# Kernel tuning notes

Hardware: AMD Instinct MI355X
Metric: run time of the kernel (lower is better)

## Reference

```python
import jax, jax.numpy as jnp
import numpy as np

B, P, D = 128, 196, 2048      # batch, num_pixels (14*14), encoder_dim
A, E, H, V = 512, 512, 512, 10000  # attention_dim, embedding_size, lstm_size, vocab
T_MAX = 20
T = T_MAX - 1                 # decoder steps = max_length - 1


def setup_inputs() -> dict:
    key = jax.random.key(0)
    ks = jax.random.split(key, 24)
    s = lambda k, sh: (jax.random.normal(k, sh, jnp.float32) * 0.02)
    features = jax.random.normal(ks[0], (B, P, D), jnp.float32)
    captions = jax.random.randint(ks[1], (B, T_MAX), 0, V)
    # sorted-descending ragged lengths in [4, T_MAX]; force max to T_MAX
    lengths = jnp.sort(jax.random.randint(ks[2], (B,), 4, T_MAX + 1))[::-1].at[0].set(T_MAX)
    return dict(
        features=features, captions=captions, lengths=lengths,
        emb=s(ks[3], (V, E)),
        h_fc_w=s(ks[4], (D, H)), h_fc_b=jnp.zeros((H,), jnp.float32),
        c_fc_w=s(ks[5], (D, H)), c_fc_b=jnp.zeros((H,), jnp.float32),
        enc_w=s(ks[6], (D, A)), enc_b=jnp.zeros((A,), jnp.float32),
        dec_w=s(ks[7], (H, A)), dec_b=jnp.zeros((A,), jnp.float32),
        att_w=s(ks[8], (A, 1)), att_b=jnp.zeros((1,), jnp.float32),
        beta_w=s(ks[9], (H, D)), beta_b=jnp.zeros((D,), jnp.float32),
        w_ih=s(ks[10], (D + E, 4 * H)), b_ih=jnp.zeros((4 * H,), jnp.float32),
        w_hh=s(ks[11], (H, 4 * H)), b_hh=jnp.zeros((4 * H,), jnp.float32),
        cls_w=s(ks[12], (H, V)), cls_b=jnp.zeros((V,), jnp.float32),
    )


def reference(features, captions, lengths, emb,
              h_fc_w, h_fc_b, c_fc_w, c_fc_b,
              enc_w, enc_b, dec_w, dec_b, att_w, att_b,
              beta_w, beta_b, w_ih, b_ih, w_hh, b_hh, cls_w, cls_b):
    dec_len = lengths - 1                       # decoder_lengths
    mean_f = features.mean(axis=1)              # [B, D]
    h = mean_f @ h_fc_w + h_fc_b                # [B, H]
    c = mean_f @ c_fc_w + c_fc_b
    att1 = features @ enc_w + enc_b             # [B, P, A] (loop-invariant)
    emb_seq = emb[captions[:, :T]]              # [B, T, E]
    xs = (jnp.moveaxis(emb_seq, 0, 1),          # [T, B, E]
          jnp.arange(T)[:, None] < dec_len[None, :])  # [T, B] step-valid mask

    def step(carry, x):
        h, c = carry
        e_t, m = x                              # [B, E], [B] bool
        att2 = h @ dec_w + dec_b                # [B, A]
        e = jnp.squeeze(jax.nn.relu(att1 + att2[:, None, :]) @ att_w + att_b, -1)  # [B, P]
        alpha = jax.nn.softmax(e, axis=1)
        awe = jnp.einsum('bp,bpd->bd', alpha, features)
        gate = jax.nn.sigmoid(h @ beta_w + beta_b)
        awe = gate * awe
        xin = jnp.concatenate([e_t, awe], axis=1)           # [B, E+D]
        gates = xin @ w_ih + b_ih + h @ w_hh + b_hh         # [B, 4H]
        i, f, g, o = jnp.split(gates, 4, axis=1)
        c_new = jax.nn.sigmoid(f) * c + jax.nn.sigmoid(i) * jnp.tanh(g)
        h_new = jax.nn.sigmoid(o) * jnp.tanh(c_new)
        mf = m[:, None].astype(h.dtype)
        y = (h_new @ cls_w + cls_b) * mf        # rows past their length stay 0
        h = jnp.where(m[:, None], h_new, h)
        c = jnp.where(m[:, None], c_new, c)
        return (h, c), (y, alpha * mf)

    _, (ys, alphas) = jax.lax.scan(step, (h, c), xs)
    y_predicted = jnp.moveaxis(ys, 0, 1)        # [B, T, V]
    alphas = jnp.moveaxis(alphas, 0, 1)         # [B, T, P]
    return y_predicted, alphas
```

## Files before the change

### kernel.cpp

```cpp
#include <hip/hip_runtime.h>
#include <cstdint>
#include <cstddef>


#define DEV __device__ __forceinline__

typedef __attribute__((ext_vector_type(8))) short s16x8;
typedef __attribute__((ext_vector_type(4))) float f32x4;

constexpr int Bb = 128, Pp = 196, Dd = 2048, Aa = 512, Ee = 512, Hh = 512, Vv = 10000;
constexpr int Tt = 19, TMAX = 20;
constexpr int KXN = 2560;
constexpr int NVP = 10048;

DEV float fbs(short s) {
    union { uint32_t u; float f; } v;
    v.u = ((uint32_t)(uint16_t)s) << 16;
    return v.f;
}
DEV short bfs(float f) {
    union { float f; uint32_t u; } v;
    v.f = f;
    uint32_t u = v.u;
    uint32_t r = (u + 0x7FFFu + ((u >> 16) & 1u)) >> 16;
    return (short)(uint16_t)r;
}

template<int BM, int BN, int BK, int WR, int WC>
DEV void tile_mm(const short* __restrict__ Ag, int lda,
                 const short* __restrict__ Bg, int ldb, int K,
                 int m0, int n0, char* smem,
                 f32x4 (&acc)[(BM / WR) / 16][(BN / WC) / 16])
{
    constexpr int TH = 256;
    constexpr int NCH = BK / 8, AU = NCH * BM, BU = NCH * BN;
    constexpr int APT = AU / TH, BPT = BU / TH;
    constexpr int WM = BM / WR, WN = BN / WC, FM = WM / 16, FN = WN / 16;
    short* sA = (short*)smem;
    short* sB = (short*)smem + AU * 8;
    const int tid = threadIdx.x, lane = tid & 63, wid = tid >> 6;
    const int l15 = lane & 15, l4 = lane >> 4, wr = wid / WC, wc = wid % WC;

    #pragma unroll
    for (int i = 0; i < FM; ++i)
        #pragma unroll
        for (int j = 0; j < FN; ++j) acc[i][j] = {0.f, 0.f, 0.f, 0.f};

    for (int kt = 0; kt < K; kt += BK) {
        s16x8 ra[APT], rb[BPT];
        #pragma unroll
        for (int i = 0; i < APT; ++i) {
            int q2 = tid + TH * i;
            int r2 = q2 / NCH, ch = q2 % NCH;
            ra[i] = *(const s16x8*)(Ag + (size_t)(m0 + r2) * lda + kt + ch * 8);
        }
        #pragma unroll
        for (int i = 0; i < BPT; ++i) {
            int q2 = tid + TH * i;
            int r2 = q2 / NCH, ch = q2 % NCH;
            rb[i] = *(const s16x8*)(Bg + (size_t)(n0 + r2) * ldb + kt + ch * 8);
        }
        __syncthreads();
        #pragma unroll
        for (int i = 0; i < APT; ++i) {
            int q2 = tid + TH * i;
            int r2 = q2 / NCH, ch = q2 % NCH;
            *(s16x8*)(sA + (r2 * NCH + (ch ^ (r2 & 7))) * 8) = ra[i];
        }
        #pragma unroll
        for (int i = 0; i < BPT; ++i) {
            int q2 = tid + TH * i;
            int r2 = q2 / NCH, ch = q2 % NCH;
            *(s16x8*)(sB + (r2 * NCH + (ch ^ (r2 & 7))) * 8) = rb[i];
        }
        __syncthreads();
        #pragma unroll
        for (int ks = 0; ks < BK / 32; ++ks) {
            s16x8 af[FM], bf[FN];
            #pragma unroll
            for (int fm = 0; fm < FM; ++fm) {
                int rr2 = wr * WM + fm * 16 + l15, cc = ks * 4 + l4;
                af[fm] = *(const s16x8*)&sA[(rr2 * NCH + (cc ^ (rr2 & 7))) * 8];
            }
            #pragma unroll
            for (int fn = 0; fn < FN; ++fn) {
                int rr2 = wc * WN + fn * 16 + l15, cc = ks * 4 + l4;
                bf[fn] = *(const s16x8*)&sB[(rr2 * NCH + (cc ^ (rr2 & 7))) * 8];
            }
            #pragma unroll
            for (int fm = 0; fm < FM; ++fm)
                #pragma unroll
                for (int fn = 0; fn < FN; ++fn)
                    acc[fm][fn] = __builtin_amdgcn_mfma_f32_16x16x32_bf16(af[fm], bf[fn], acc[fm][fn], 0, 0, 0);
        }
        __syncthreads();
    }
}

template<int BM, int BN, int BK, int TH, int WR, int WC, int EPI>
__global__ __launch_bounds__(TH) void gemm_k(
    const short* __restrict__ Ag, int lda,
    const short* __restrict__ Bg, int ldb,
    int K,
    float* __restrict__ outF, float* __restrict__ outF2,
    short* __restrict__ outH, short* __restrict__ outH2,
    int ldo,
    const float* __restrict__ bias, const float* __restrict__ bias2,
    const int* __restrict__ lens)
{
    constexpr int NCH = BK / 8;
    constexpr int AU = NCH * BM, BU = NCH * BN;
    constexpr int APT = AU / TH, BPT = BU / TH;
    constexpr int WM = BM / WR, WN = BN / WC;
    constexpr int FM = WM / 16, FN = WN / 16;

    __shared__ __align__(16) short sA[AU * 8];
    __shared__ __align__(16) short sB[BU * 8];

    const int tid = threadIdx.x, lane = tid & 63, wid = tid >> 6;
    const int l15 = lane & 15, l4 = lane >> 4;

    int m0, n0, trow_ = 0;
    if constexpr (EPI == 0) {
        int task = (blockIdx.x & 7) * 49 + (blockIdx.x >> 3);
        m0 = (task >> 1) * BM;
        n0 = (task & 1) * BN;
    } else if constexpr (EPI == 3) {
        const int nwg = (int)gridDim.x;
        const int qq = nwg >> 3, rr = nwg & 7;
        int xcd = (int)blockIdx.x & 7, idx = (int)blockIdx.x >> 3;
        int task = (xcd < rr) ? xcd * (qq + 1) + idx
                              : rr * (qq + 1) + (xcd - rr) * qq + idx;
        int npanel = task / Tt;
        trow_ = task - npanel * Tt;
        m0 = trow_ * BM;
        n0 = npanel * BN;
    } else if constexpr (EPI == 4) {
        m0 = ((int)blockIdx.x & 3) * BM;
        n0 = ((int)blockIdx.x >> 2) * BN;
    } else {
        m0 = blockIdx.y * BM;
        n0 = blockIdx.x * BN;
    }
    const int wr = wid / WC, wc = wid % WC;

    f32x4 acc[FM][FN];
    #pragma unroll
    for (int i = 0; i < FM; ++i)
        #pragma unroll
        for (int j = 0; j < FN; ++j) acc[i][j] = {0.f, 0.f, 0.f, 0.f};

    for (int kt = 0; kt < K; kt += BK) {
        s16x8 ra[APT], rb[BPT];
        #pragma unroll
        for (int i = 0; i < APT; ++i) {
            int q2 = tid + TH * i;
            int r2 = q2 / NCH, ch = q2 % NCH;
            ra[i] = *(const s16x8*)(Ag + (size_t)(m0 + r2) * lda + kt + ch * 8);
        }
        #pragma unroll
        for (int i = 0; i < BPT; ++i) {
            int q2 = tid + TH * i;
            int r2 = q2 / NCH, ch = q2 % NCH;
            rb[i] = *(const s16x8*)(Bg + (size_t)(n0 + r2) * ldb + kt + ch * 8);
        }
        __syncthreads();
        #pragma unroll
        for (int i = 0; i < APT; ++i) {
            int q2 = tid + TH * i;
            int r2 = q2 / NCH, ch = q2 % NCH;
            *(s16x8*)(sA + (r2 * NCH + (ch ^ (r2 & 7))) * 8) = ra[i];
        }
        #pragma unroll
        for (int i = 0; i < BPT; ++i) {
            int q2 = tid + TH * i;
            int r2 = q2 / NCH, ch = q2 % NCH;
            *(s16x8*)(sB + (r2 * NCH + (ch ^ (r2 & 7))) * 8) = rb[i];
        }
        __syncthreads();
        #pragma unroll
        for (int ks = 0; ks < BK / 32; ++ks) {
            s16x8 af[FM], bf[FN];
            #pragma unroll
            for (int fm = 0; fm < FM; ++fm) {
                int rr2 = wr * WM + fm * 16 + l15, cc = ks * 4 + l4;
                af[fm] = *(const s16x8*)&sA[(rr2 * NCH + (cc ^ (rr2 & 7))) * 8];
            }
            #pragma unroll
            for (int fn = 0; fn < FN; ++fn) {
                int rr2 = wc * WN + fn * 16 + l15, cc = ks * 4 + l4;
                bf[fn] = *(const s16x8*)&sB[(rr2 * NCH + (cc ^ (rr2 & 7))) * 8];
            }
            #pragma unroll
            for (int fm = 0; fm < FM; ++fm)
                #pragma unroll
                for (int fn = 0; fn < FN; ++fn)
                    acc[fm][fn] = __builtin_amdgcn_mfma_f32_16x16x32_bf16(af[fm], bf[fn], acc[fm][fn], 0, 0, 0);
        }
        __syncthreads();
    }

    #pragma unroll
    for (int fm = 0; fm < FM; ++fm)
        #pragma unroll
        for (int fn = 0; fn < FN; ++fn)
            #pragma unroll
            for (int r2 = 0; r2 < 4; ++r2) {
                int ml = wr * WM + fm * 16 + l4 * 4 + r2;
                int nl = wc * WN + fn * 16 + l15;
                int m = m0 + ml, n = n0 + nl;
                float v = acc[fm][fn][r2];
                if constexpr (EPI == 0) {
                    outH[(size_t)m * ldo + n] = bfs(v + bias[n]);
                } else if constexpr (EPI == 1) {
                    outH[(size_t)m * ldo + n] = bfs(v);
                } else if constexpr (EPI == 3) {
                    if (n < Vv) {
                        bool mk = trow_ < lens[ml] - 1;
                        outF[((size_t)ml * Tt + trow_) * Vv + n] = mk ? (v + bias[n]) : 0.f;
                    }
                } else if constexpr (EPI == 4) {
                    if (n < 512) outF[(size_t)m * Aa + n] = v + bias[n];
                    else outF2[(size_t)m * Dd + (n - 512)] =
                             1.f / (1.f + expf(-(v + bias2[n - 512])));
                } else if constexpr (EPI == 6) {
                    if (n < 512) {
                        outH2[(size_t)m * KXN + 2048 + n] = bfs(v + bias[n]);
                    } else {
                        outF2[(size_t)m * 512 + (n - 512)] = v + bias2[n - 512];
                    }
                }
            }
}

__global__ __launch_bounds__(512) void att_awe_k(
    const short* __restrict__ att1b, const float* __restrict__ att2b,
    const float* __restrict__ att_w, const float* __restrict__ att_b,
    const short* __restrict__ featb, const float* __restrict__ gatebuf,
    short* __restrict__ xin, float* __restrict__ al_out,
    const int* __restrict__ lens, int t)
{
    const int b = blockIdx.y, half = blockIdx.x;
    const int tid = threadIdx.x, lane = tid & 63, wid = tid >> 6;
    __shared__ float se[224];
    __shared__ float sred[256];
    __shared__ float sal[224];

    float aw[8], a2[8];
    #pragma unroll
    for (int j = 0; j < 8; ++j) {
        aw[j] = att_w[lane * 8 + j];
        a2[j] = att2b[b * 512 + lane * 8 + j];
    }
    float ab = att_b[0];
    for (int p = wid; p < Pp; p += 8) {
        s16x8 row = *(const s16x8*)&att1b[((size_t)b * Pp + p) * 512 + lane * 8];
        float s = 0.f;
        #pragma unroll
        for (int j = 0; j < 8; ++j) {
            float v = fbs(row[j]) + a2[j];
            v = v > 0.f ? v : 0.f;
            s += v * aw[j];
        }
        #pragma unroll
        for (int m = 32; m; m >>= 1) s += __shfl_xor(s, m);
        if (lane == 0) se[p] = s + ab;
    }
    __syncthreads();
    float e = 0.f, ex = 0.f;
    if (tid < 256) {
        e = (tid < Pp) ? se[tid] : -3.0e38f;
        sred[tid] = e;
    }
    __syncthreads();
    for (int st = 128; st > 0; st >>= 1) {
        if (tid < st) sred[tid] = fmaxf(sred[tid], sred[tid + st]);
        __syncthreads();
    }
    float mx = sred[0];
    __syncthreads();
    if (tid < 256) {
        ex = (tid < Pp) ? expf(e - mx) : 0.f;
        sred[tid] = ex;
    }
    __syncthreads();
    for (int st = 128; st > 0; st >>= 1) {
        if (tid < st) sred[tid] += sred[tid + st];
        __syncthreads();
    }
    float inv = 1.f / sred[0];
    if (tid < Pp) {
        float al = ex * inv;
        sal[tid] = al;
        if (half == 0) {
            float mf = (t < lens[b] - 1) ? 1.f : 0.f;
            al_out[((size_t)b * Tt + t) * Pp + tid] = al * mf;
        }
    }
    __syncthreads();
    int d0 = half * 1024 + tid * 2;
    const short* f = featb + (size_t)b * Pp * Dd + d0;
    float s0 = 0.f, s1 = 0.f;
    #pragma unroll 4
    for (int p = 0; p < Pp; ++p) {
        uint32_t v = *(const uint32_t*)(f + (size_t)p * Dd);
        float al = sal[p];
        s0 += al * fbs((short)(v & 0xFFFF));
        s1 += al * fbs((short)(v >> 16));
    }
    float2 g = *(const float2*)&gatebuf[b * 2048 + d0];
    uint32_t o = ((uint32_t)(uint16_t)bfs(g.y * s1) << 16) | (uint16_t)bfs(g.x * s0);
    *(uint32_t*)(xin + (size_t)b * KXN + d0) = o;
}

__global__ __launch_bounds__(256) void gates_lstm_k(
    const short* __restrict__ xin, const short* __restrict__ combT,
    const short* __restrict__ eprec,
    const float* __restrict__ b_ih, const float* __restrict__ b_hh,
    float* __restrict__ c_state, short* __restrict__ hnew_all,
    short* __restrict__ xin_h, const int* __restrict__ lens, int t)
{
    __shared__ __align__(16) char smem[16384];
    int m0 = ((int)blockIdx.x & 3) * 32, n0 = ((int)blockIdx.x >> 2) * 32;
    f32x4 acc[1][1];
    tile_mm<32, 32, 128, 2, 2>(xin, KXN, combT, KXN, KXN, m0, n0, smem, acc);
    int tid = threadIdx.x, lane = tid & 63, wid = tid >> 6;
    int l15 = lane & 15, l4 = lane >> 4, wr = wid / 2, wc = wid % 2;
    float* sE = (float*)smem;
    #pragma unroll
    for (int r = 0; r < 4; ++r) {
        int ml = wr * 16 + l4 * 4 + r, nl = wc * 16 + l15;
        sE[ml * 32 + nl] = acc[0][0][r];
    }
    __syncthreads();
    int bl = tid >> 3, jl = tid & 7;
    int b = m0 + bl, q = (n0 >> 2) + jl;
    f32x4 ge = *(const f32x4*)&sE[bl * 32 + jl * 4];
    short4 ep = *(const short4*)&eprec[((size_t)t * 128 + b) * 2048 + n0 + jl * 4];
    float gi = ge[0] + fbs(ep.x) + b_ih[q]        + b_hh[q];
    float gf = ge[1] + fbs(ep.y) + b_ih[512 + q]  + b_hh[512 + q];
    float gg = ge[2] + fbs(ep.z) + b_ih[1024 + q] + b_hh[1024 + q];
    float go = ge[3] + fbs(ep.w) + b_ih[1536 + q] + b_hh[1536 + q];
    float si = 1.f / (1.f + expf(-gi));
    float sf = 1.f / (1.f + expf(-gf));
    float so = 1.f / (1.f + expf(-go));
    float tg = tanhf(gg);
    int sidx = b * 512 + q;
    float cn = sf * c_state[sidx] + si * tg;
    float hn = so * tanhf(cn);
    hnew_all[((size_t)t * 128 + b) * 512 + q] = bfs(hn);
    if (t < lens[b] - 1) {
        c_state[sidx] = cn;
        xin_h[(size_t)b * KXN + 2048 + q] = bfs(hn);
    }
}

__global__ __launch_bounds__(256) void conv_mean_k(
    const float* __restrict__ feat, short* __restrict__ featb, short* __restrict__ meanb)
{
    int b = blockIdx.y;
    int d = (blockIdx.x * 256 + threadIdx.x) * 4;
    const float* f = feat + (size_t)b * Pp * Dd + d;
    short* o = featb + (size_t)b * Pp * Dd + d;
    float s0 = 0.f, s1 = 0.f, s2 = 0.f, s3 = 0.f;
    for (int p = 0; p < Pp; ++p) {
        float4 v = *(const float4*)(f + (size_t)p * Dd);
        s0 += v.x; s1 += v.y; s2 += v.z; s3 += v.w;
        short4 ov = make_short4(bfs(v.x), bfs(v.y), bfs(v.z), bfs(v.w));
        *(short4*)(o + (size_t)p * Dd) = ov;
    }
    const float inv = 1.f / 196.f;
    short4 mv = make_short4(bfs(s0 * inv), bfs(s1 * inv), bfs(s2 * inv), bfs(s3 * inv));
    *(short4*)(meanb + (size_t)b * Dd + d) = mv;
}

template<int PERM>
__global__ __launch_bounds__(256) void transpose_bf16(
    const float* __restrict__ src, int R, int C,
    short* __restrict__ dst, int dstStride, int colOff, int Cpad)
{
    __shared__ float tile[32][33];
    int c0 = blockIdx.x * 32, r0 = blockIdx.y * 32;
    int tx = threadIdx.x & 31, ty = threadIdx.x >> 5;
    #pragma unroll
    for (int i = 0; i < 4; ++i) {
        int r = r0 + ty + i * 8, c = c0 + tx;
        tile[ty + i * 8][tx] = (r < R && c < C) ? src[(size_t)r * C + c] : 0.f;
    }
    __syncthreads();
    #pragma unroll
    for (int i = 0; i < 4; ++i) {
        int cc = c0 + ty + i * 8, rr = r0 + tx;
        if (cc < Cpad && rr < R) {
            int drow = PERM ? ((cc & 511) * 4 + (cc >> 9)) : cc;
            dst[(size_t)drow * dstStride + colOff + rr] = bfs(tile[tx][ty + i * 8]);
        }
    }
}

__global__ __launch_bounds__(256) void embg_k(
    const float* __restrict__ emb, const int* __restrict__ caps, short* __restrict__ embseq)
{
    size_t i = (size_t)blockIdx.x * 256 + threadIdx.x;
    if (i >= (size_t)Tt * Bb * Ee) return;
    int e = (int)(i % Ee);
    size_t r = i / Ee;
    int b = (int)(r % Bb);
    int t = (int)(r / Bb);
    int cap = caps[b * TMAX + t];
    embseq[i] = bfs(emb[(size_t)cap * Ee + e]);
}

extern "C" void kernel_launch(void* const* d_in, const int* in_sizes, int n_in,
                              void* d_out, int out_size, void* d_ws, size_t ws_size,
                              hipStream_t stream)
{
    const float* features = (const float*)d_in[0];
    const int* captions   = (const int*)d_in[1];
    const int* lengths    = (const int*)d_in[2];
    const float* emb      = (const float*)d_in[3];
    const float* h_fc_w   = (const float*)d_in[4];
    const float* h_fc_b   = (const float*)d_in[5];
    const float* c_fc_w   = (const float*)d_in[6];
    const float* c_fc_b   = (const float*)d_in[7];
    const float* enc_w    = (const float*)d_in[8];
    const float* enc_b    = (const float*)d_in[9];
    const float* dec_w    = (const float*)d_in[10];
    const float* dec_b    = (const float*)d_in[11];
    const float* att_w    = (const float*)d_in[12];
    const float* att_b    = (const float*)d_in[13];
    const float* beta_w   = (const float*)d_in[14];
    const float* beta_b   = (const float*)d_in[15];
    const float* w_ih     = (const float*)d_in[16];
    const float* b_ih     = (const float*)d_in[17];
    const float* w_hh     = (const float*)d_in[18];
    const float* b_hh     = (const float*)d_in[19];
    const float* cls_w    = (const float*)d_in[20];
    const float* cls_b    = (const float*)d_in[21];

    char* w = (char*)d_ws;
    auto alloc = [&](size_t bytes) {
        char* p = w;
        w += (bytes + 255) & ~(size_t)255;
        return p;
    };
    short* featb    = (short*)alloc((size_t)Bb * Pp * Dd * 2);
    short* att1b    = (short*)alloc((size_t)Bb * Pp * Aa * 2);
    short* encT     = (short*)alloc((size_t)Aa * Dd * 2);
    short* combT    = (short*)alloc((size_t)2048 * KXN * 2);
    short* wtopT    = (short*)alloc((size_t)2048 * 512 * 2);
    short* clsT     = (short*)alloc((size_t)NVP * Hh * 2);
    short* catT     = (short*)alloc((size_t)2560 * Hh * 2);
    short* hcT      = (short*)alloc((size_t)1024 * Dd * 2);
    short* embseq   = (short*)alloc((size_t)Tt * Bb * Ee * 2);
    short* meanb    = (short*)alloc((size_t)Bb * Dd * 2);
    short* eprec    = (short*)alloc((size_t)Tt * Bb * 2048 * 2);
    float* c_state  = (float*)alloc((size_t)Bb * Hh * 4);
    float* att2b    = (float*)alloc((size_t)Bb * Aa * 4);
    float* gatebuf  = (float*)alloc((size_t)Bb * Dd * 4);
    short* xin      = (short*)alloc((size_t)Bb * KXN * 2);
    short* hnew_all = (short*)alloc((size_t)Tt * Bb * Hh * 2);

    float* y_out  = (float*)d_out;
    float* al_out = y_out + (size_t)Bb * Tt * Vv;

    conv_mean_k<<<dim3(2, 128), 256, 0, stream>>>(features, featb, meanb);
    transpose_bf16<0><<<dim3(16, 64), 256, 0, stream>>>(enc_w, 2048, 512, encT, 2048, 0, 512);
    transpose_bf16<0><<<dim3(16, 64), 256, 0, stream>>>(h_fc_w, 2048, 512, hcT, 2048, 0, 512);
    transpose_bf16<0><<<dim3(16, 64), 256, 0, stream>>>(c_fc_w, 2048, 512, hcT + (size_t)512 * 2048, 2048, 0, 512);
    transpose_bf16<0><<<dim3(16, 16), 256, 0, stream>>>(dec_w, 512, 512, catT, 512, 0, 512);
    transpose_bf16<0><<<dim3(64, 16), 256, 0, stream>>>(beta_w, 512, 2048, catT + (size_t)512 * 512, 512, 0, 2048);
    transpose_bf16<1><<<dim3(64, 64), 256, 0, stream>>>(w_ih + (size_t)512 * 2048, 2048, 2048, combT, KXN, 0, 2048);
    transpose_bf16<1><<<dim3(64, 16), 256, 0, stream>>>(w_hh, 512, 2048, combT, KXN, 2048, 2048);
    transpose_bf16<1><<<dim3(64, 16), 256, 0, stream>>>(w_ih, 512, 2048, wtopT, 512, 0, 2048);
    transpose_bf16<0><<<dim3(314, 16), 256, 0, stream>>>(cls_w, 512, 10000, clsT, 512, 0, NVP);
    embg_k<<<(Tt * Bb * Ee + 255) / 256, 256, 0, stream>>>(emb, captions, embseq);

    gemm_k<128, 64, 64, 256, 2, 2, 6><<<dim3(16, 1), 256, 0, stream>>>(
        meanb, 2048, hcT, 2048, 2048,
        nullptr, c_state, nullptr, xin, 0, h_fc_b, c_fc_b, nullptr);

    gemm_k<128, 256, 64, 512, 2, 4, 0><<<dim3(392), 512, 0, stream>>>(
        featb, 2048, encT, 2048, 2048,
        nullptr, nullptr, att1b, nullptr, Aa, enc_b, nullptr, nullptr);

    gemm_k<128, 64, 64, 256, 2, 2, 1><<<dim3(32, 19), 256, 0, stream>>>(
        embseq, 512, wtopT, 512, 512,
        nullptr, nullptr, eprec, nullptr, 2048, nullptr, nullptr, nullptr);

    for (int t = 0; t < Tt; ++t) {
        gemm_k<32, 64, 64, 256, 2, 2, 4><<<dim3(160), 256, 0, stream>>>(
            xin + 2048, KXN, catT, 512, 512,
            att2b, gatebuf, nullptr, nullptr, 0, dec_b, beta_b, nullptr);
        att_awe_k<<<dim3(2, 128), 512, 0, stream>>>(
            att1b, att2b, att_w, att_b, featb, gatebuf, xin,
            al_out, lengths, t);
        gates_lstm_k<<<dim3(256), 256, 0, stream>>>(
            xin, combT, eprec, b_ih, b_hh, c_state, hnew_all, xin, lengths, t);
    }

    gemm_k<128, 64, 64, 256, 2, 2, 3><<<dim3(157 * Tt), 256, 0, stream>>>(
        hnew_all, 512, clsT, 512, 512,
        y_out, nullptr, nullptr, nullptr, 0, cls_b, nullptr, lengths);
}
```

Before: 1.475 ms.

## Fuse att2/gate GEMV into attention kernel, merge prep transposes, pipeline LSTM GEMM

The per-step att2/beta-gate GEMM launch is removed. Each attention block now computes its own h·dec_w and sigmoid(h·beta_w) slice as a scalar GEMV from the bf16 weights, cutting one launch per step and the att2/gate round trip through global memory. In exchange, each of the two half-blocks per batch row recomputes the full att2 vector, and every block reads weight rows redundantly. The LSTM gates GEMM gets a hand-written double-buffered register prefetch. The many weight-transpose and embedding-gather launches are merged into a single prep kernel, and the feature conversion now uses narrower per-thread vectors across more blocks.

```diff
diff --git a/kernel.cpp b/kernel.cpp
--- a/kernel.cpp
+++ b/kernel.cpp
@@ -7,6 +7,7 @@
 
 typedef __attribute__((ext_vector_type(8))) short s16x8;
 typedef __attribute__((ext_vector_type(4))) float f32x4;
+typedef __attribute__((ext_vector_type(4))) unsigned int u32x4;
 
 constexpr int Bb = 128, Pp = 196, Dd = 2048, Aa = 512, Ee = 512, Hh = 512, Vv = 10000;
 constexpr int Tt = 19, TMAX = 20;
@@ -25,76 +26,12 @@
     uint32_t r = (u + 0x7FFFu + ((u >> 16) & 1u)) >> 16;
     return (short)(uint16_t)r;
 }
-
-template<int BM, int BN, int BK, int WR, int WC>
-DEV void tile_mm(const short* __restrict__ Ag, int lda,
-                 const short* __restrict__ Bg, int ldb, int K,
-                 int m0, int n0, char* smem,
-                 f32x4 (&acc)[(BM / WR) / 16][(BN / WC) / 16])
-{
-    constexpr int TH = 256;
-    constexpr int NCH = BK / 8, AU = NCH * BM, BU = NCH * BN;
-    constexpr int APT = AU / TH, BPT = BU / TH;
-    constexpr int WM = BM / WR, WN = BN / WC, FM = WM / 16, FN = WN / 16;
-    short* sA = (short*)smem;
-    short* sB = (short*)smem + AU * 8;
-    const int tid = threadIdx.x, lane = tid & 63, wid = tid >> 6;
-    const int l15 = lane & 15, l4 = lane >> 4, wr = wid / WC, wc = wid % WC;
-
-    #pragma unroll
-    for (int i = 0; i < FM; ++i)
-        #pragma unroll
-        for (int j = 0; j < FN; ++j) acc[i][j] = {0.f, 0.f, 0.f, 0.f};
-
-    for (int kt = 0; kt < K; kt += BK) {
-        s16x8 ra[APT], rb[BPT];
-        #pragma unroll
-        for (int i = 0; i < APT; ++i) {
-            int q2 = tid + TH * i;
-            int r2 = q2 / NCH, ch = q2 % NCH;
-            ra[i] = *(const s16x8*)(Ag + (size_t)(m0 + r2) * lda + kt + ch * 8);
-        }
-        #pragma unroll
-        for (int i = 0; i < BPT; ++i) {
-            int q2 = tid + TH * i;
-            int r2 = q2 / NCH, ch = q2 % NCH;
-            rb[i] = *(const s16x8*)(Bg + (size_t)(n0 + r2) * ldb + kt + ch * 8);
-        }
-        __syncthreads();
-        #pragma unroll
-        for (int i = 0; i < APT; ++i) {
-            int q2 = tid + TH * i;
-            int r2 = q2 / NCH, ch = q2 % NCH;
-            *(s16x8*)(sA + (r2 * NCH + (ch ^ (r2 & 7))) * 8) = ra[i];
-        }
-        #pragma unroll
-        for (int i = 0; i < BPT; ++i) {
-            int q2 = tid + TH * i;
-            int r2 = q2 / NCH, ch = q2 % NCH;
-            *(s16x8*)(sB + (r2 * NCH + (ch ^ (r2 & 7))) * 8) = rb[i];
-        }
-        __syncthreads();
-        #pragma unroll
-        for (int ks = 0; ks < BK / 32; ++ks) {
-            s16x8 af[FM], bf[FN];
-            #pragma unroll
-            for (int fm = 0; fm < FM; ++fm) {
-                int rr2 = wr * WM + fm * 16 + l15, cc = ks * 4 + l4;
-                af[fm] = *(const s16x8*)&sA[(rr2 * NCH + (cc ^ (rr2 & 7))) * 8];
-            }
-            #pragma unroll
-            for (int fn = 0; fn < FN; ++fn) {
-                int rr2 = wc * WN + fn * 16 + l15, cc = ks * 4 + l4;
-                bf[fn] = *(const s16x8*)&sB[(rr2 * NCH + (cc ^ (rr2 & 7))) * 8];
-            }
-            #pragma unroll
-            for (int fm = 0; fm < FM; ++fm)
-                #pragma unroll
-                for (int fn = 0; fn < FN; ++fn)
-                    acc[fm][fn] = __builtin_amdgcn_mfma_f32_16x16x32_bf16(af[fm], bf[fn], acc[fm][fn], 0, 0, 0);
-        }
-        __syncthreads();
-    }
+DEV void upk(uint32_t v, float& lo, float& hi) {
+    union { uint32_t u; float f; } a, b;
+    a.u = v << 16;
+    b.u = v & 0xffff0000u;
+    lo = a.f;
+    hi = b.f;
 }
 
 template<int BM, int BN, int BK, int TH, int WR, int WC, int EPI>
@@ -135,9 +72,6 @@
         trow_ = task - npanel * Tt;
         m0 = trow_ * BM;
         n0 = npanel * BN;
-    } else if constexpr (EPI == 4) {
-        m0 = ((int)blockIdx.x & 3) * BM;
-        n0 = ((int)blockIdx.x >> 2) * BN;
     } else {
         m0 = blockIdx.y * BM;
         n0 = blockIdx.x * BN;
@@ -219,10 +153,6 @@
                         bool mk = trow_ < lens[ml] - 1;
                         outF[((size_t)ml * Tt + trow_) * Vv + n] = mk ? (v + bias[n]) : 0.f;
                     }
-                } else if constexpr (EPI == 4) {
-                    if (n < 512) outF[(size_t)m * Aa + n] = v + bias[n];
-                    else outF2[(size_t)m * Dd + (n - 512)] =
-                             1.f / (1.f + expf(-(v + bias2[n - 512])));
                 } else if constexpr (EPI == 6) {
                     if (n < 512) {
                         outH2[(size_t)m * KXN + 2048 + n] = bfs(v + bias[n]);
@@ -234,83 +164,124 @@
 }
 
 __global__ __launch_bounds__(512) void att_awe_k(
-    const short* __restrict__ att1b, const float* __restrict__ att2b,
+    const short* __restrict__ att1b, const short* __restrict__ catT,
+    const float* __restrict__ dec_b, const float* __restrict__ beta_b,
     const float* __restrict__ att_w, const float* __restrict__ att_b,
-    const short* __restrict__ featb, const float* __restrict__ gatebuf,
-    short* __restrict__ xin, float* __restrict__ al_out,
-    const int* __restrict__ lens, int t)
+    const short* __restrict__ featb, short* __restrict__ xin,
+    float* __restrict__ al_out, const int* __restrict__ lens, int t)
 {
     const int b = blockIdx.y, half = blockIdx.x;
     const int tid = threadIdx.x, lane = tid & 63, wid = tid >> 6;
+    __shared__ float sh[512];
+    __shared__ float sa2[512];
     __shared__ float se[224];
     __shared__ float sred[256];
     __shared__ float sal[224];
 
-    float aw[8], a2[8];
-    #pragma unroll
-    for (int j = 0; j < 8; ++j) {
-        aw[j] = att_w[lane * 8 + j];
-        a2[j] = att2b[b * 512 + lane * 8 + j];
-    }
-    float ab = att_b[0];
-    for (int p = wid; p < Pp; p += 8) {
-        s16x8 row = *(const s16x8*)&att1b[((size_t)b * Pp + p) * 512 + lane * 8];
-        float s = 0.f;
+    if (tid < 256) {
+        uint32_t v = ((const uint32_t*)(xin + (size_t)b * KXN + 2048))[tid];
+        float lo, hi;
+        upk(v, lo, hi);
+        sh[tid * 2] = lo;
+        sh[tid * 2 + 1] = hi;
+    }
+    __syncthreads();
+
+    const int d0 = half * 1024 + tid * 2;
+    {
+        const short* wa = catT + (size_t)tid * 512;
+        const short* w0 = catT + (size_t)(512 + d0) * 512;
+        const short* w1 = w0 + 512;
+        float accA = 0.f, acc0 = 0.f, acc1 = 0.f;
+        #pragma unroll 4
+        for (int k = 0; k < 512; k += 8) {
+            u32x4 va = *(const u32x4*)(wa + k);
+            u32x4 v0 = *(const u32x4*)(w0 + k);
+            u32x4 v1 = *(const u32x4*)(w1 + k);
+            float hv[8];
+            *(float4*)&hv[0] = *(const float4*)&sh[k];
+            *(float4*)&hv[4] = *(const float4*)&sh[k + 4];
+            #pragma unroll
+            for (int j = 0; j < 4; ++j) {
+                float lo, hi;
+                upk(va[j], lo, hi); accA += lo * hv[2 * j] + hi * hv[2 * j + 1];
+                upk(v0[j], lo, hi); acc0 += lo * hv[2 * j] + hi * hv[2 * j + 1];
+                upk(v1[j], lo, hi); acc1 += lo * hv[2 * j] + hi * hv[2 * j + 1];
+            }
+        }
+        sa2[tid] = accA + dec_b[tid];
+        float g0 = 1.f / (1.f + expf(-(acc0 + beta_b[d0])));
+        float g1 = 1.f / (1.f + expf(-(acc1 + beta_b[d0 + 1])));
+        __syncthreads();
+
+        float aw[8], a2[8];
         #pragma unroll
         for (int j = 0; j < 8; ++j) {
-            float v = fbs(row[j]) + a2[j];
-            v = v > 0.f ? v : 0.f;
-            s += v * aw[j];
-        }
-        #pragma unroll
-        for (int m = 32; m; m >>= 1) s += __shfl_xor(s, m);
-        if (lane == 0) se[p] = s + ab;
-    }
-    __syncthreads();
-    float e = 0.f, ex = 0.f;
-    if (tid < 256) {
-        e = (tid < Pp) ? se[tid] : -3.0e38f;
-        sred[tid] = e;
-    }
-    __syncthreads();
-    for (int st = 128; st > 0; st >>= 1) {
-        if (tid < st) sred[tid] = fmaxf(sred[tid], sred[tid + st]);
-        __syncthreads();
-    }
-    float mx = sred[0];
-    __syncthreads();
-    if (tid < 256) {
-        ex = (tid < Pp) ? expf(e - mx) : 0.f;
-        sred[tid] = ex;
-    }
-    __syncthreads();
-    for (int st = 128; st > 0; st >>= 1) {
-        if (tid < st) sred[tid] += sred[tid + st];
-        __syncthreads();
-    }
-    float inv = 1.f / sred[0];
-    if (tid < Pp) {
-        float al = ex * inv;
-        sal[tid] = al;
-        if (half == 0) {
-            float mf = (t < lens[b] - 1) ? 1.f : 0.f;
-            al_out[((size_t)b * Tt + t) * Pp + tid] = al * mf;
-        }
-    }
-    __syncthreads();
-    int d0 = half * 1024 + tid * 2;
-    const short* f = featb + (size_t)b * Pp * Dd + d0;
-    float s0 = 0.f, s1 = 0.f;
-    #pragma unroll 4
-    for (int p = 0; p < Pp; ++p) {
-        uint32_t v = *(const uint32_t*)(f + (size_t)p * Dd);
-        float al = sal[p];
-        s0 += al * fbs((short)(v & 0xFFFF));
-        s1 += al * fbs((short)(v >> 16));
-    }
-    float2 g = *(const float2*)&gatebuf[b * 2048 + d0];
-    uint32_t o = ((uint32_t)(uint16_t)bfs(g.y * s1) << 16) | (uint16_t)bfs(g.x * s0);
-    *(uint32_t*)(xin + (size_t)b * KXN + d0) = o;
+            aw[j] = att_w[lane * 8 + j];
+            a2[j] = sa2[lane * 8 + j];
+        }
+        float ab = att_b[0];
+        for (int p = wid; p < Pp; p += 8) {
+            s16x8 row = *(const s16x8*)&att1b[((size_t)b * Pp + p) * 512 + lane * 8];
+            float s = 0.f;
+            #pragma unroll
+            for (int j = 0; j < 8; ++j) {
+                float v = fbs(row[j]) + a2[j];
+                v = v > 0.f ? v : 0.f;
+                s += v * aw[j];
+            }
+            #pragma unroll
+            for (int m = 32; m; m >>= 1) s += __shfl_xor(s, m);
+            if (lane == 0) se[p] = s + ab;
+        }
+        __syncthreads();
+
+        float e = 0.f, ex = 0.f;
+        if (tid < 256) {
+            e = (tid < Pp) ? se[tid] : -3.0e38f;
+            sred[tid] = e;
+        }
+        __syncthreads();
+        for (int st = 128; st > 0; st >>= 1) {
+            if (tid < st) sred[tid] = fmaxf(sred[tid], sred[tid + st]);
+            __syncthreads();
+        }
+        float mx = sred[0];
+        __syncthreads();
+        if (tid < 256) {
+            ex = (tid < Pp) ? expf(e - mx) : 0.f;
+            sred[tid] = ex;
+        }
+        __syncthreads();
+        for (int st = 128; st > 0; st >>= 1) {
+            if (tid < st) sred[tid] += sred[tid + st];
+            __syncthreads();
+        }
+        float inv = 1.f / sred[0];
+        if (tid < Pp) {
+            float al = ex * inv;
+            sal[tid] = al;
+            if (half == 0) {
+                float mf = (t < lens[b] - 1) ? 1.f : 0.f;
+                al_out[((size_t)b * Tt + t) * Pp + tid] = al * mf;
+            }
+        }
+        __syncthreads();
+
+        const short* f = featb + (size_t)b * Pp * Dd + d0;
+        float s0 = 0.f, s1 = 0.f;
+        #pragma unroll 4
+        for (int p = 0; p < Pp; ++p) {
+            uint32_t v = *(const uint32_t*)(f + (size_t)p * Dd);
+            float lo, hi;
+            upk(v, lo, hi);
+            float al = sal[p];
+            s0 += al * lo;
+            s1 += al * hi;
+        }
+        uint32_t o = ((uint32_t)(uint16_t)bfs(g1 * s1) << 16) | (uint16_t)bfs(g0 * s0);
+        *(uint32_t*)(xin + (size_t)b * KXN + d0) = o;
+    }
 }
 
 __global__ __launch_bounds__(256) void gates_lstm_k(
@@ -320,17 +291,71 @@
     float* __restrict__ c_state, short* __restrict__ hnew_all,
     short* __restrict__ xin_h, const int* __restrict__ lens, int t)
 {
-    __shared__ __align__(16) char smem[16384];
-    int m0 = ((int)blockIdx.x & 3) * 32, n0 = ((int)blockIdx.x >> 2) * 32;
-    f32x4 acc[1][1];
-    tile_mm<32, 32, 128, 2, 2>(xin, KXN, combT, KXN, KXN, m0, n0, smem, acc);
-    int tid = threadIdx.x, lane = tid & 63, wid = tid >> 6;
-    int l15 = lane & 15, l4 = lane >> 4, wr = wid / 2, wc = wid % 2;
-    float* sE = (float*)smem;
+    constexpr int BM = 32, BN = 32, BK = 128, K = KXN;
+    constexpr int NCH = BK / 8;
+    constexpr int AU = NCH * BM;
+    __shared__ __align__(16) short sA[AU * 8];
+    __shared__ __align__(16) short sB[AU * 8];
+
+    const int m0 = ((int)blockIdx.x & 3) * BM, n0 = ((int)blockIdx.x >> 2) * BN;
+    const int tid = threadIdx.x, lane = tid & 63, wid = tid >> 6;
+    const int l15 = lane & 15, l4 = lane >> 4;
+    const int wr = wid >> 1, wc = wid & 1;
+
+    f32x4 acc = {0.f, 0.f, 0.f, 0.f};
+    const int r2 = tid / NCH, ch0 = tid % NCH;
+    const short* Abase = xin + (size_t)(m0 + r2) * KXN + ch0 * 8;
+    const short* Bbase = combT + (size_t)(n0 + r2) * KXN + ch0 * 8;
+    const size_t rowadv = (size_t)16 * KXN;
+
+    s16x8 raA0, raA1, rbA0, rbA1, raB0, raB1, rbB0, rbB1;
+
+    auto loadA = [&](int kt, s16x8& a0, s16x8& a1, s16x8& b0, s16x8& b1) {
+        a0 = *(const s16x8*)(Abase + kt);
+        a1 = *(const s16x8*)(Abase + rowadv + kt);
+        b0 = *(const s16x8*)(Bbase + kt);
+        b1 = *(const s16x8*)(Bbase + rowadv + kt);
+    };
+    const int sl0 = ((r2) * NCH + (ch0 ^ (r2 & 7))) * 8;
+    const int sl1 = ((r2 + 16) * NCH + (ch0 ^ ((r2 + 16) & 7))) * 8;
+    auto storeS = [&](s16x8& a0, s16x8& a1, s16x8& b0, s16x8& b1) {
+        *(s16x8*)(sA + sl0) = a0;
+        *(s16x8*)(sA + sl1) = a1;
+        *(s16x8*)(sB + sl0) = b0;
+        *(s16x8*)(sB + sl1) = b1;
+    };
+    const int rrA = wr * 16 + l15, rrB = wc * 16 + l15;
+    auto mfmaS = [&]() {
+        #pragma unroll
+        for (int ks = 0; ks < BK / 32; ++ks) {
+            int cc = ks * 4 + l4;
+            s16x8 af = *(const s16x8*)&sA[(rrA * NCH + (cc ^ (rrA & 7))) * 8];
+            s16x8 bf = *(const s16x8*)&sB[(rrB * NCH + (cc ^ (rrB & 7))) * 8];
+            acc = __builtin_amdgcn_mfma_f32_16x16x32_bf16(af, bf, acc, 0, 0, 0);
+        }
+    };
+
+    loadA(0, raA0, raA1, rbA0, rbA1);
+    #pragma unroll 1
+    for (int kt = 0; kt < K; kt += 2 * BK) {
+        __syncthreads();
+        storeS(raA0, raA1, rbA0, rbA1);
+        __syncthreads();
+        if (kt + BK < K) loadA(kt + BK, raB0, raB1, rbB0, rbB1);
+        mfmaS();
+        __syncthreads();
+        storeS(raB0, raB1, rbB0, rbB1);
+        __syncthreads();
+        if (kt + 2 * BK < K) loadA(kt + 2 * BK, raA0, raA1, rbA0, rbA1);
+        mfmaS();
+    }
+
+    __syncthreads();
+    float* sE = (float*)sA;
     #pragma unroll
     for (int r = 0; r < 4; ++r) {
         int ml = wr * 16 + l4 * 4 + r, nl = wc * 16 + l15;
-        sE[ml * 32 + nl] = acc[0][0][r];
+        sE[ml * 32 + nl] = acc[r];
     }
     __syncthreads();
     int bl = tid >> 3, jl = tid & 7;
@@ -359,28 +384,28 @@
     const float* __restrict__ feat, short* __restrict__ featb, short* __restrict__ meanb)
 {
     int b = blockIdx.y;
-    int d = (blockIdx.x * 256 + threadIdx.x) * 4;
+    int d = (blockIdx.x * 256 + threadIdx.x) * 2;
     const float* f = feat + (size_t)b * Pp * Dd + d;
     short* o = featb + (size_t)b * Pp * Dd + d;
-    float s0 = 0.f, s1 = 0.f, s2 = 0.f, s3 = 0.f;
+    float s0 = 0.f, s1 = 0.f;
+    #pragma unroll 4
     for (int p = 0; p < Pp; ++p) {
-        float4 v = *(const float4*)(f + (size_t)p * Dd);
-        s0 += v.x; s1 += v.y; s2 += v.z; s3 += v.w;
-        short4 ov = make_short4(bfs(v.x), bfs(v.y), bfs(v.z), bfs(v.w));
-        *(short4*)(o + (size_t)p * Dd) = ov;
+        float2 v = *(const float2*)(f + (size_t)p * Dd);
+        s0 += v.x; s1 += v.y;
+        uint32_t ov = ((uint32_t)(uint16_t)bfs(v.y) << 16) | (uint16_t)bfs(v.x);
+        *(uint32_t*)(o + (size_t)p * Dd) = ov;
     }
     const float inv = 1.f / 196.f;
-    short4 mv = make_short4(bfs(s0 * inv), bfs(s1 * inv), bfs(s2 * inv), bfs(s3 * inv));
-    *(short4*)(meanb + (size_t)b * Dd + d) = mv;
-}
-
-template<int PERM>
-__global__ __launch_bounds__(256) void transpose_bf16(
-    const float* __restrict__ src, int R, int C,
-    short* __restrict__ dst, int dstStride, int colOff, int Cpad)
-{
-    __shared__ float tile[32][33];
-    int c0 = blockIdx.x * 32, r0 = blockIdx.y * 32;
+    uint32_t mv = ((uint32_t)(uint16_t)bfs(s1 * inv) << 16) | (uint16_t)bfs(s0 * inv);
+    *(uint32_t*)(meanb + (size_t)b * Dd + d) = mv;
+}
+
+DEV void t32(const float* __restrict__ src, int R, int C,
+             short* __restrict__ dst, int ds, int off, int perm,
+             int local, int gx, float (*tile)[33])
+{
+    int x = local % gx, y = local / gx;
+    int c0 = x * 32, r0 = y * 32;
     int tx = threadIdx.x & 31, ty = threadIdx.x >> 5;
     #pragma unroll
     for (int i = 0; i < 4; ++i) {
@@ -391,24 +416,45 @@
     #pragma unroll
     for (int i = 0; i < 4; ++i) {
         int cc = c0 + ty + i * 8, rr = r0 + tx;
-        if (cc < Cpad && rr < R) {
-            int drow = PERM ? ((cc & 511) * 4 + (cc >> 9)) : cc;
-            dst[(size_t)drow * dstStride + colOff + rr] = bfs(tile[tx][ty + i * 8]);
-        }
-    }
-}
-
-__global__ __launch_bounds__(256) void embg_k(
-    const float* __restrict__ emb, const int* __restrict__ caps, short* __restrict__ embseq)
-{
-    size_t i = (size_t)blockIdx.x * 256 + threadIdx.x;
-    if (i >= (size_t)Tt * Bb * Ee) return;
-    int e = (int)(i % Ee);
-    size_t r = i / Ee;
-    int b = (int)(r % Bb);
-    int t = (int)(r / Bb);
-    int cap = caps[b * TMAX + t];
-    embseq[i] = bfs(emb[(size_t)cap * Ee + e]);
+        if (rr < R) {
+            int drow = perm ? ((cc & 511) * 4 + (cc >> 9)) : cc;
+            dst[(size_t)drow * ds + off + rr] = bfs(tile[tx][ty + i * 8]);
+        }
+    }
+}
+
+__global__ __launch_bounds__(256) void prep_k(
+    const float* __restrict__ enc_w, const float* __restrict__ h_fc_w,
+    const float* __restrict__ c_fc_w, const float* __restrict__ dec_w,
+    const float* __restrict__ beta_w, const float* __restrict__ w_ih,
+    const float* __restrict__ w_hh, const float* __restrict__ cls_w,
+    const float* __restrict__ emb, const int* __restrict__ caps,
+    short* __restrict__ encT, short* __restrict__ hcT, short* __restrict__ catT,
+    short* __restrict__ combT, short* __restrict__ wtopT, short* __restrict__ clsT,
+    short* __restrict__ embseq)
+{
+    __shared__ float tile[32][33];
+    int bid = blockIdx.x;
+    if (bid < 1024)        t32(enc_w, 2048, 512, encT, 2048, 0, 0, bid, 16, tile);
+    else if (bid < 2048)   t32(h_fc_w, 2048, 512, hcT, 2048, 0, 0, bid - 1024, 16, tile);
+    else if (bid < 3072)   t32(c_fc_w, 2048, 512, hcT + (size_t)512 * 2048, 2048, 0, 0, bid - 2048, 16, tile);
+    else if (bid < 3328)   t32(dec_w, 512, 512, catT, 512, 0, 0, bid - 3072, 16, tile);
+    else if (bid < 4352)   t32(beta_w, 512, 2048, catT + (size_t)512 * 512, 512, 0, 0, bid - 3328, 64, tile);
+    else if (bid < 8448)   t32(w_ih + (size_t)512 * 2048, 2048, 2048, combT, KXN, 0, 1, bid - 4352, 64, tile);
+    else if (bid < 9472)   t32(w_hh, 512, 2048, combT, KXN, 2048, 1, bid - 8448, 64, tile);
+    else if (bid < 10496)  t32(w_ih, 512, 2048, wtopT, 512, 0, 1, bid - 9472, 64, tile);
+    else if (bid < 15520)  t32(cls_w, 512, 10000, clsT, 512, 0, 0, bid - 10496, 314, tile);
+    else {
+        size_t i = (size_t)(bid - 15520) * 256 + threadIdx.x;
+        if (i < (size_t)Tt * Bb * Ee) {
+            int e = (int)(i % Ee);
+            size_t r = i / Ee;
+            int b = (int)(r % Bb);
+            int t = (int)(r / Bb);
+            int cap = caps[b * TMAX + t];
+            embseq[i] = bfs(emb[(size_t)cap * Ee + e]);
+        }
+    }
 }
 
 extern "C" void kernel_launch(void* const* d_in, const int* in_sizes, int n_in,
@@ -456,25 +502,16 @@
     short* meanb    = (short*)alloc((size_t)Bb * Dd * 2);
     short* eprec    = (short*)alloc((size_t)Tt * Bb * 2048 * 2);
     float* c_state  = (float*)alloc((size_t)Bb * Hh * 4);
-    float* att2b    = (float*)alloc((size_t)Bb * Aa * 4);
-    float* gatebuf  = (float*)alloc((size_t)Bb * Dd * 4);
     short* xin      = (short*)alloc((size_t)Bb * KXN * 2);
     short* hnew_all = (short*)alloc((size_t)Tt * Bb * Hh * 2);
 
     float* y_out  = (float*)d_out;
     float* al_out = y_out + (size_t)Bb * Tt * Vv;
 
-    conv_mean_k<<<dim3(2, 128), 256, 0, stream>>>(features, featb, meanb);
-    transpose_bf16<0><<<dim3(16, 64), 256, 0, stream>>>(enc_w, 2048, 512, encT, 2048, 0, 512);
-    transpose_bf16<0><<<dim3(16, 64), 256, 0, stream>>>(h_fc_w, 2048, 512, hcT, 2048, 0, 512);
-    transpose_bf16<0><<<dim3(16, 64), 256, 0, stream>>>(c_fc_w, 2048, 512, hcT + (size_t)512 * 2048, 2048, 0, 512);
-    transpose_bf16<0><<<dim3(16, 16), 256, 0, stream>>>(dec_w, 512, 512, catT, 512, 0, 512);
-    transpose_bf16<0><<<dim3(64, 16), 256, 0, stream>>>(beta_w, 512, 2048, catT + (size_t)512 * 512, 512, 0, 2048);
-    transpose_bf16<1><<<dim3(64, 64), 256, 0, stream>>>(w_ih + (size_t)512 * 2048, 2048, 2048, combT, KXN, 0, 2048);
-    transpose_bf16<1><<<dim3(64, 16), 256, 0, stream>>>(w_hh, 512, 2048, combT, KXN, 2048, 2048);
-    transpose_bf16<1><<<dim3(64, 16), 256, 0, stream>>>(w_ih, 512, 2048, wtopT, 512, 0, 2048);
-    transpose_bf16<0><<<dim3(314, 16), 256, 0, stream>>>(cls_w, 512, 10000, clsT, 512, 0, NVP);
-    embg_k<<<(Tt * Bb * Ee + 255) / 256, 256, 0, stream>>>(emb, captions, embseq);
+    conv_mean_k<<<dim3(4, 128), 256, 0, stream>>>(features, featb, meanb);
+    prep_k<<<dim3(20384), 256, 0, stream>>>(
+        enc_w, h_fc_w, c_fc_w, dec_w, beta_w, w_ih, w_hh, cls_w, emb, captions,
+        encT, hcT, catT, combT, wtopT, clsT, embseq);
 
     gemm_k<128, 64, 64, 256, 2, 2, 6><<<dim3(16, 1), 256, 0, stream>>>(
         meanb, 2048, hcT, 2048, 2048,
@@ -489,11 +526,8 @@
         nullptr, nullptr, eprec, nullptr, 2048, nullptr, nullptr, nullptr);
 
     for (int t = 0; t < Tt; ++t) {
-        gemm_k<32, 64, 64, 256, 2, 2, 4><<<dim3(160), 256, 0, stream>>>(
-            xin + 2048, KXN, catT, 512, 512,
-            att2b, gatebuf, nullptr, nullptr, 0, dec_b, beta_b, nullptr);
         att_awe_k<<<dim3(2, 128), 512, 0, stream>>>(
-            att1b, att2b, att_w, att_b, featb, gatebuf, xin,
+            att1b, catT, dec_b, beta_b, att_w, att_b, featb, xin,
             al_out, lengths, t);
         gates_lstm_k<<<dim3(256), 256, 0, stream>>>(
             xin, combT, eprec, b_ih, b_hh, c_state, hnew_all, xin, lengths, t);
```

New measurement: 2.341 ms. 58.7% more time.
